# Optimization experiments

Hardware: AMD Instinct MI355X
Metric: run time of the kernel (lower is better)

## Reference

```python
import jax, jax.numpy as jnp
import numpy as np

H = 16
QK_NOPE = 128
QK_ROPE = 64
QK_HEAD = 192
V_HEAD = 128
KV_LORA = 512
Q_LORA = 1536
HIDDEN = 2048
ROPE_THETA = 500000.0
EPS = 1e-6


def _rms_norm(x, w, eps=EPS):
    var = jnp.mean(x * x, axis=-1, keepdims=True)
    return w * (x * jax.lax.rsqrt(var + eps))


def _rotate_half(x):
    d = x.shape[-1] // 2
    return jnp.concatenate([-x[..., d:], x[..., :d]], axis=-1)


def _rope_cos_sin(T, dim, theta, dtype):
    inv_freq = 1.0 / (theta ** (jnp.arange(0, dim, 2, dtype=jnp.float32) / dim))
    t = jnp.arange(T, dtype=jnp.float32)
    freqs = jnp.outer(t, inv_freq)               # [T, dim//2]
    emb = jnp.concatenate([freqs, freqs], axis=-1)  # [T, dim]
    return jnp.cos(emb).astype(dtype), jnp.sin(emb).astype(dtype)


def _apply_rope_interleave(q, k, cos, sin):
    # deinterleave: [x0,x1,x2,...] -> [x0,x2,... , x1,x3,...]
    def deint(x):
        return jnp.concatenate([x[..., 0::2], x[..., 1::2]], axis=-1)
    q, k = deint(q), deint(k)
    cos = cos[None, None]  # [1,1,T,d]
    sin = sin[None, None]
    q_e = q * cos + _rotate_half(q) * sin
    k_e = k * cos + _rotate_half(k) * sin
    return q_e, k_e


def setup_inputs() -> dict:
    key = jax.random.key(0)
    ks = jax.random.split(key, 8)
    s = 0.02
    B, T = 2, 2048
    return {
        "x": jax.random.normal(ks[0], (B, T, HIDDEN), jnp.float32),
        "q_a_w": jax.random.normal(ks[1], (HIDDEN, Q_LORA), jnp.float32) * s,
        "q_a_ln_w": jnp.ones((Q_LORA,), jnp.float32),
        "q_b_w": jax.random.normal(ks[2], (Q_LORA, H * QK_HEAD), jnp.float32) * s,
        "kv_a_w": jax.random.normal(ks[3], (HIDDEN, KV_LORA + QK_ROPE), jnp.float32) * s,
        "kv_a_ln_w": jnp.ones((KV_LORA,), jnp.float32),
        "kv_b_w": jax.random.normal(ks[4], (KV_LORA, H * (QK_NOPE + V_HEAD)), jnp.float32) * s,
        "o_w": jax.random.normal(ks[5], (H * V_HEAD, HIDDEN), jnp.float32) * s,
    }


def reference(x, q_a_w, q_a_ln_w, q_b_w, kv_a_w, kv_a_ln_w, kv_b_w, o_w):
    B, T, _ = x.shape
    scale = QK_HEAD ** -0.5

    # Q path: hidden -> q_lora -> RMSNorm -> H*qk_head
    q = _rms_norm(x @ q_a_w, q_a_ln_w) @ q_b_w
    q = q.reshape(B, T, H, QK_HEAD).transpose(0, 2, 1, 3)  # [B,H,T,qk_head]
    q_nope, q_rope = q[..., :QK_NOPE], q[..., QK_NOPE:]

    # KV path: hidden -> kv_lora + rope_dim
    ckv = x @ kv_a_w
    kv_c, k_rope = ckv[..., :KV_LORA], ckv[..., KV_LORA:]
    kv = _rms_norm(kv_c, kv_a_ln_w) @ kv_b_w
    kv = kv.reshape(B, T, H, QK_NOPE + V_HEAD).transpose(0, 2, 1, 3)
    k_nope, v = kv[..., :QK_NOPE], kv[..., QK_NOPE:]

    k_rope = k_rope.reshape(B, 1, T, QK_ROPE)
    cos, sin = _rope_cos_sin(T, QK_ROPE, ROPE_THETA, x.dtype)
    q_rope, k_rope = _apply_rope_interleave(q_rope, k_rope, cos, sin)
    k_rope = jnp.broadcast_to(k_rope, (B, H, T, QK_ROPE))

    qf = jnp.concatenate([q_nope, q_rope], axis=-1)  # [B,H,T,192]
    kf = jnp.concatenate([k_nope, k_rope], axis=-1)

    # causal SDPA
    scores = jnp.einsum("bhqd,bhkd->bhqk", qf, kf) * scale
    causal = jnp.tril(jnp.ones((T, T), bool))
    scores = jnp.where(causal[None, None], scores, jnp.finfo(scores.dtype).min)
    attn = jax.nn.softmax(scores, axis=-1)
    out = jnp.einsum("bhqk,bhkd->bhqd", attn, v)  # [B,H,T,128]
    out = out.transpose(0, 2, 1, 3).reshape(B, T, H * V_HEAD)
    return out @ o_w
```

## Files before the change

### kernel.cpp

```cpp
#include <hip/hip_runtime.h>
#include <hip/hip_bf16.h>
#include <cstdint>


typedef __bf16 bf16;
typedef __bf16 bf16x8 __attribute__((ext_vector_type(8)));
typedef __bf16 bf16x4v __attribute__((ext_vector_type(4)));
typedef float f32x4 __attribute__((ext_vector_type(4)));

#define TSEQ 2048
#define MR 4096

typedef const uint32_t __attribute__((address_space(1))) * gas1_t;
typedef uint32_t __attribute__((address_space(3))) * las3_t;

static __device__ __forceinline__ void gload_lds16(const void* g, void* l) {
  __builtin_amdgcn_global_load_lds(
      reinterpret_cast<gas1_t>(reinterpret_cast<uintptr_t>(g)),
      reinterpret_cast<las3_t>(reinterpret_cast<uintptr_t>(l)), 16, 0, 0);
}

static __device__ __forceinline__ f32x4 mfma16(bf16x8 a, bf16x8 b, f32x4 c) {
  return __builtin_amdgcn_mfma_f32_16x16x32_bf16(a, b, c, 0, 0, 0);
}

static __device__ __forceinline__ void do_transpose(
    const float* __restrict__ W, bf16* __restrict__ Wt, int K, int N, int bi,
    int bj, float (*t)[33]) {
  int c = threadIdx.x & 31, r0 = threadIdx.x >> 5;
#pragma unroll
  for (int rr = 0; rr < 32; rr += 8)
    t[rr + r0][c] = W[(size_t)(bj * 32 + rr + r0) * N + bi * 32 + c];
  __syncthreads();
#pragma unroll
  for (int rr = 0; rr < 32; rr += 8)
    Wt[(size_t)(bi * 32 + rr + r0) * K + bj * 32 + c] = (bf16)t[c][rr + r0];
}

#define PREP_BLOCKS (8192 + 3072 + 1152 + 4608 + 2048 + 4096 + 192 + 256)

__global__ __launch_bounds__(256) void k_prep(
    const float* __restrict__ x, const float* __restrict__ q_a_w,
    const float* __restrict__ kv_a_w, const float* __restrict__ q_b_w,
    const float* __restrict__ kv_b_w, const float* __restrict__ o_w,
    bf16* __restrict__ x_bf, bf16* __restrict__ ab_wt,
    bf16* __restrict__ qb_wt, bf16* __restrict__ kvb_wt,
    bf16* __restrict__ o_wt, float* __restrict__ rt) {
  __shared__ float t[32][33];
  int nb = blockIdx.x;
  const int tid = threadIdx.x;
  if (nb < 8192) {
    int i = nb * 256 + tid;
    float4 f = reinterpret_cast<const float4*>(x)[i];
    bf16x4v o = {(bf16)f.x, (bf16)f.y, (bf16)f.z, (bf16)f.w};
    reinterpret_cast<bf16x4v*>(x_bf)[i] = o;
    return;
  }
  nb -= 8192;
  if (nb < 3072) { do_transpose(q_a_w, ab_wt, 2048, 1536, nb % 48, nb / 48, t); return; }
  nb -= 3072;
  if (nb < 1152) {
    do_transpose(kv_a_w, ab_wt + (size_t)1536 * 2048, 2048, 576, nb % 18, nb / 18, t);
    return;
  }
  nb -= 1152;
  if (nb < 4608) { do_transpose(q_b_w, qb_wt, 1536, 3072, nb % 96, nb / 96, t); return; }
  nb -= 4608;
  if (nb < 2048) { do_transpose(kv_b_w, kvb_wt, 512, 4096, nb % 128, nb / 128, t); return; }
  nb -= 2048;
  if (nb < 4096) { do_transpose(o_w, o_wt, 2048, 2048, nb % 64, nb / 64, t); return; }
  nb -= 4096;
  if (nb < 192) {
    uint4 z = make_uint4(0, 0, 0, 0);
    reinterpret_cast<uint4*>(ab_wt + (size_t)2112 * 2048)[nb * 256 + tid] = z;
    return;
  }
  nb -= 192;
  {
    int idx = nb * 256 + tid;
    int tt = idx >> 5, j = idx & 31;
    float freq = exp2f(-(float)j * (1.0f / 32.0f) * log2f(500000.0f));
    float ang = (float)tt * freq;
    rt[tt * 64 + 2 * j] = cosf(ang);
    rt[tt * 64 + 2 * j + 1] = sinf(ang);
  }
}

__global__ __launch_bounds__(64) void k_norms(
    const bf16* __restrict__ qac, const float* __restrict__ qw,
    const float* __restrict__ kvw, const float* __restrict__ rt,
    bf16* __restrict__ q_a_n, bf16* __restrict__ kv_c_n,
    bf16* __restrict__ kr) {
  int row = blockIdx.x, lane = threadIdx.x;
  const bf16* ip = qac + (size_t)row * 2304;
  bf16x8 v[3];
  float ss = 0.f;
#pragma unroll
  for (int c = 0; c < 3; ++c) {
    v[c] = *reinterpret_cast<const bf16x8*>(ip + c * 512 + lane * 8);
#pragma unroll
    for (int e = 0; e < 8; ++e) { float f = (float)v[c][e]; ss += f * f; }
  }
#pragma unroll
  for (int m = 1; m <= 32; m <<= 1) ss += __shfl_xor(ss, m);
  float rs = rsqrtf(ss / 1536.0f + 1e-6f);
  bf16* op = q_a_n + (size_t)row * 1536;
#pragma unroll
  for (int c = 0; c < 3; ++c) {
    bf16x8 o;
#pragma unroll
    for (int e = 0; e < 8; ++e)
      o[e] = (bf16)((float)v[c][e] * rs * qw[c * 512 + lane * 8 + e]);
    *reinterpret_cast<bf16x8*>(op + c * 512 + lane * 8) = o;
  }
  bf16x8 kvv = *reinterpret_cast<const bf16x8*>(ip + 1536 + lane * 8);
  float s2 = 0.f;
#pragma unroll
  for (int e = 0; e < 8; ++e) { float f = (float)kvv[e]; s2 += f * f; }
#pragma unroll
  for (int m = 1; m <= 32; m <<= 1) s2 += __shfl_xor(s2, m);
  float rs2 = rsqrtf(s2 / 512.0f + 1e-6f);
  bf16x8 o2;
#pragma unroll
  for (int e = 0; e < 8; ++e)
    o2[e] = (bf16)((float)kvv[e] * rs2 * kvw[lane * 8 + e]);
  *reinterpret_cast<bf16x8*>(kv_c_n + (size_t)row * 512 + lane * 8) = o2;
  if (lane < 32) {
    int t = row & (TSEQ - 1);
    float x0 = (float)ip[2048 + 2 * lane], x1 = (float)ip[2048 + 2 * lane + 1];
    float c = rt[t * 64 + 2 * lane], s = rt[t * 64 + 2 * lane + 1];
    kr[(size_t)row * 64 + lane] = (bf16)(x0 * c - x1 * s);
    kr[(size_t)row * 64 + 32 + lane] = (bf16)(x1 * c + x0 * s);
  }
}

#define GPH(BUF, MH, KH, DO_READB, STAGE_STMT, WAIT_STMT)                     \
  {                                                                           \
    if (DO_READB) {                                                           \
      _Pragma("unroll") for (int ni = 0; ni < 4; ++ni) {                      \
        int row = wn * 64 + ni * 16 + lr;                                     \
        breg[KH][ni] = *reinterpret_cast<const bf16x8*>(                      \
            &Bs[BUF][row * 64 + ((((KH)*4 + lg) ^ (row & 7)) * 8)]);          \
      }                                                                       \
    }                                                                         \
    bf16x8 af[4];                                                             \
    _Pragma("unroll") for (int mi = 0; mi < 4; ++mi) {                        \
      int row = wm * 128 + (MH)*64 + mi * 16 + lr;                            \
      af[mi] = *reinterpret_cast<const bf16x8*>(                              \
          &As[BUF][row * 64 + ((((KH)*4 + lg) ^ (row & 7)) * 8)]);            \
    }                                                                         \
    STAGE_STMT;                                                               \
    __builtin_amdgcn_s_barrier();                                             \
    __builtin_amdgcn_s_setprio(1);                                            \
    _Pragma("unroll") for (int mi = 0; mi < 4; ++mi)                          \
        _Pragma("unroll") for (int ni = 0; ni < 4; ++ni)                      \
            acc[(MH)*4 + mi][ni] =                                            \
        mfma16(af[mi], breg[KH][ni], acc[(MH)*4 + mi][ni]);                   \
    __builtin_amdgcn_s_setprio(0);                                            \
    WAIT_STMT;                                                                \
    __builtin_amdgcn_s_barrier();                                             \
  }

template <bool OUT_F32>
static __device__ __forceinline__ void gemm8_body(
    const bf16* __restrict__ A, const bf16* __restrict__ Bt,
    void* __restrict__ C, int N, int K, int bi, int bj, bf16 (*As)[16384],
    bf16 (*Bs)[16384]) {
  const int tid = threadIdx.x, lane = tid & 63, w = tid >> 6;
  const int lg = lane >> 4, lr = lane & 15;
  const int wm = w >> 2, wn = w & 3;
  const int m0 = bj * 256, n0 = bi * 256;
  const int T = K >> 7;

  f32x4 acc[8][4] = {};
  bf16x8 breg[2][4];

  auto stageA = [&](int tau, int h) {
    char* dst = (char*)&As[tau & 1][0] + h * 16384;
#pragma unroll
    for (int j = 0; j < 2; ++j) {
      int c = j * 512 + tid;
      int row = c >> 3, slot = c & 7;
      gload_lds16(A + (size_t)(m0 + h * 128 + row) * K + tau * 64 +
                      ((slot ^ (row & 7)) * 8),
                  dst + (size_t)(j * 512 + w * 64) * 16);
    }
  };
  auto stageB = [&](int tau, int h) {
    char* dst = (char*)&Bs[tau & 1][0] + h * 16384;
#pragma unroll
    for (int j = 0; j < 2; ++j) {
      int c = j * 512 + tid;
      int row = c >> 3, slot = c & 7;
      gload_lds16(Bt + (size_t)(n0 + h * 128 + row) * K + tau * 64 +
                      ((slot ^ (row & 7)) * 8),
                  dst + (size_t)(j * 512 + w * 64) * 16);
    }
  };

  stageB(0, 0); stageB(0, 1); stageA(0, 0); stageA(0, 1);
  stageB(1, 0); stageB(1, 1); stageA(1, 0);
  asm volatile("s_waitcnt vmcnt(6)" ::: "memory");
  __builtin_amdgcn_s_barrier();

  for (int t = 0; t < T - 1; ++t) {
    const int s2 = 2 * t + 2, s3 = 2 * t + 3, a1 = 2 * t + 1;
    GPH(0, 0, 0, true,  stageA(a1, 1), ((void)0));
    GPH(0, 0, 1, true,  stageB(s2, 0), ((void)0));
    GPH(0, 1, 0, false, stageB(s2, 1), ((void)0));
    GPH(0, 1, 1, false, stageA(s2, 0),
        asm volatile("s_waitcnt vmcnt(6)" ::: "memory"));
    GPH(1, 0, 0, true,  stageA(s2, 1), ((void)0));
    GPH(1, 0, 1, true,  stageB(s3, 0), ((void)0));
    GPH(1, 1, 0, false, stageB(s3, 1), ((void)0));
    GPH(1, 1, 1, false, stageA(s3, 0),
        asm volatile("s_waitcnt vmcnt(6)" ::: "memory"));
  }
  {
    const int a1 = 2 * T - 1;
    GPH(0, 0, 0, true,  stageA(a1, 1), ((void)0));
    GPH(0, 0, 1, true,  ((void)0),     ((void)0));
    GPH(0, 1, 0, false, ((void)0),     ((void)0));
    GPH(0, 1, 1, false, ((void)0),
        asm volatile("s_waitcnt vmcnt(0)" ::: "memory"));
    GPH(1, 0, 0, true,  ((void)0), ((void)0));
    GPH(1, 0, 1, true,  ((void)0), ((void)0));
    GPH(1, 1, 0, false, ((void)0), ((void)0));
    GPH(1, 1, 1, false, ((void)0), ((void)0));
  }

#pragma unroll
  for (int mi = 0; mi < 8; ++mi)
#pragma unroll
    for (int ni = 0; ni < 4; ++ni) {
      int col = n0 + wn * 64 + ni * 16 + lr;
#pragma unroll
      for (int r = 0; r < 4; ++r) {
        int rowg = m0 + wm * 128 + mi * 16 + lg * 4 + r;
        if (OUT_F32)
          reinterpret_cast<float*>(C)[(size_t)rowg * N + col] = acc[mi][ni][r];
        else
          reinterpret_cast<bf16*>(C)[(size_t)rowg * N + col] =
              (bf16)acc[mi][ni][r];
      }
    }
}

template <bool OUT_F32>
__global__ __launch_bounds__(512, 2) void k_gemm8(const bf16* __restrict__ A,
                                                  const bf16* __restrict__ Bt,
                                                  void* __restrict__ C, int N,
                                                  int K) {
  __shared__ bf16 As[2][16384];
  __shared__ bf16 Bs[2][16384];
  const int nwg = gridDim.x * gridDim.y;
  const int orig = blockIdx.y * gridDim.x + blockIdx.x;
  const int wgid = (orig & 7) * (nwg >> 3) + (orig >> 3);
  gemm8_body<OUT_F32>(A, Bt, C, N, K, wgid % gridDim.x, wgid / gridDim.x, As,
                      Bs);
}

__global__ __launch_bounds__(512, 2) void k_gemm8_dual(
    const bf16* __restrict__ A1, const bf16* __restrict__ B1,
    bf16* __restrict__ C1, const bf16* __restrict__ A2,
    const bf16* __restrict__ B2, bf16* __restrict__ C2) {
  __shared__ bf16 As[2][16384];
  __shared__ bf16 Bs[2][16384];
  int id = blockIdx.x;
  if (id < 192) {
    int wg = (id & 7) * 24 + (id >> 3);
    gemm8_body<false>(A1, B1, C1, 3072, 1536, wg % 12, wg / 12, As, Bs);
  } else {
    int s = id - 192;
    int wg = (s & 7) * 32 + (s >> 3);
    gemm8_body<false>(A2, B2, C2, 4096, 512, wg % 16, wg / 16, As, Bs);
  }
}

#define GPN(BUF, KH, STAGE_STMT, WAIT_STMT)                                   \
  {                                                                           \
    bf16x8 bfr[4];                                                            \
    _Pragma("unroll") for (int ni = 0; ni < 4; ++ni) {                        \
      int row = wn * 64 + ni * 16 + lr;                                       \
      bfr[ni] = *reinterpret_cast<const bf16x8*>(                             \
          &Bs[BUF][row * 64 + ((((KH)*4 + lg) ^ (row & 7)) * 8)]);            \
    }                                                                         \
    bf16x8 af[4];                                                             \
    _Pragma("unroll") for (int mi = 0; mi < 4; ++mi) {                        \
      int row = wm * 64 + mi * 16 + lr;                                       \
      af[mi] = *reinterpret_cast<const bf16x8*>(                              \
          &As[BUF][row * 64 + ((((KH)*4 + lg) ^ (row & 7)) * 8)]);            \
    }                                                                         \
    STAGE_STMT;                                                               \
    __builtin_amdgcn_s_barrier();                                             \
    __builtin_amdgcn_s_setprio(1);                                            \
    _Pragma("unroll") for (int mi = 0; mi < 4; ++mi)                          \
        _Pragma("unroll") for (int ni = 0; ni < 4; ++ni)                      \
            acc[mi][ni] = mfma16(af[mi], bfr[ni], acc[mi][ni]);               \
    __builtin_amdgcn_s_setprio(0);                                            \
    WAIT_STMT;                                                                \
    __builtin_amdgcn_s_barrier();                                             \
  }

template <bool OUT_F32>
__global__ __launch_bounds__(512, 2) void k_gemm4n(const bf16* __restrict__ A,
                                                   const bf16* __restrict__ Bt,
                                                   void* __restrict__ C, int N,
                                                   int K) {
  __shared__ bf16 As[2][16384];
  __shared__ bf16 Bs[2][8192];
  const int tid = threadIdx.x, lane = tid & 63, w = tid >> 6;
  const int lg = lane >> 4, lr = lane & 15;
  const int wm = w >> 1, wn = w & 1;
  const int nwg = gridDim.x * gridDim.y;
  const int orig = blockIdx.y * gridDim.x + blockIdx.x;
  const int wgid = (orig & 7) * (nwg >> 3) + (orig >> 3);
  const int m0 = (wgid / gridDim.x) * 256, n0 = (wgid % gridDim.x) * 128;
  const int T = K >> 7;

  f32x4 acc[4][4] = {};

  auto stA = [&](int tau, int h) {
    char* dst = (char*)&As[tau & 1][0] + h * 16384;
#pragma unroll
    for (int j = 0; j < 2; ++j) {
      int c = j * 512 + tid;
      int row = c >> 3, slot = c & 7;
      gload_lds16(A + (size_t)(m0 + h * 128 + row) * K + tau * 64 +
                      ((slot ^ (row & 7)) * 8),
                  dst + (size_t)(j * 512 + w * 64) * 16);
    }
  };
  auto stB = [&](int tau) {
    char* dst = (char*)&Bs[tau & 1][0];
#pragma unroll
    for (int j = 0; j < 2; ++j) {
      int c = j * 512 + tid;
      int row = c >> 3, slot = c & 7;
      gload_lds16(Bt + (size_t)(n0 + row) * K + tau * 64 +
                      ((slot ^ (row & 7)) * 8),
                  dst + (size_t)(j * 512 + w * 64) * 16);
    }
  };

  stA(0, 0); stA(0, 1); stB(0); stA(1, 0);
  asm volatile("s_waitcnt vmcnt(2)" ::: "memory");
  __builtin_amdgcn_s_barrier();

  for (int t = 0; t < T - 1; ++t) {
    const int u1 = 2 * t + 1, s2 = 2 * t + 2, s3 = 2 * t + 3;
    GPN(0, 0, stA(u1, 1), ((void)0));
    GPN(0, 1, { stB(u1); stA(s2, 0); },
        asm volatile("s_waitcnt vmcnt(2)" ::: "memory"));
    GPN(1, 0, stA(s2, 1), ((void)0));
    GPN(1, 1, { stB(s2); stA(s3, 0); },
        asm volatile("s_waitcnt vmcnt(2)" ::: "memory"));
  }
  {
    const int u1 = 2 * T - 1;
    GPN(0, 0, stA(u1, 1), ((void)0));
    GPN(0, 1, stB(u1),
        asm volatile("s_waitcnt vmcnt(0)" ::: "memory"));
    GPN(1, 0, ((void)0), ((void)0));
    GPN(1, 1, ((void)0), ((void)0));
  }

#pragma unroll
  for (int mi = 0; mi < 4; ++mi)
#pragma unroll
    for (int ni = 0; ni < 4; ++ni) {
      int col = n0 + wn * 64 + ni * 16 + lr;
#pragma unroll
      for (int r = 0; r < 4; ++r) {
        int rowg = m0 + wm * 64 + mi * 16 + lg * 4 + r;
        if (OUT_F32)
          reinterpret_cast<float*>(C)[(size_t)rowg * N + col] = acc[mi][ni][r];
        else
          reinterpret_cast<bf16*>(C)[(size_t)rowg * N + col] =
              (bf16)acc[mi][ni][r];
      }
    }
}

__global__ __launch_bounds__(512, 2) void k_attn(const bf16* __restrict__ q,
                                                 const bf16* __restrict__ kv,
                                                 const bf16* __restrict__ kr,
                                                 const float* __restrict__ rt,
                                                 bf16* __restrict__ o) {
  __shared__ bf16 Kn[2][64 * 128];
  __shared__ bf16 Kr[2][64 * 64];
  __shared__ bf16 Vs[2][64 * 128];
  __shared__ bf16 Ps[8 * 1024];
  const int tid = threadIdx.x, lane = tid & 63, w = tid >> 6;
  const int lg = lane >> 4, lr = lane & 15;
  const float qsc = 0.07216878364870323f * 1.44269504088896f;
  uint4 vreg[2];
  const int vrr = tid & 31, vvc = tid >> 5;

  for (int t = 0; t < 2; ++t) {
    const int id = t ? 511 - (int)blockIdx.x : (int)blockIdx.x;
    const int qt = 15 - (id >> 5);
    const int bh = id & 31;
    const int b = bh >> 4, h = bh & 15;
    const int q0 = qt * 128;
    const size_t rowbase = (size_t)b * TSEQ;
    const int nkt = 2 * qt + 2;
    const int qg = q0 + w * 16 + lr;

    auto issue_loads = [&](int kbase, int buf) {
#pragma unroll
      for (int kk = 0; kk < 2; ++kk)
        vreg[kk] = *reinterpret_cast<const uint4*>(
            kv + (rowbase + kbase + vrr * 2 + kk) * 4096 + h * 256 + 128 +
            vvc * 8);
#pragma unroll
      for (int i = 0; i < 2; ++i) {
        int c = i * 512 + tid;
        int row = c >> 4, j = c & 15;
        gload_lds16(
            kv + (rowbase + kbase + row) * 4096 + h * 256 +
                ((j ^ (row & 15)) * 8),
            (char*)&Kn[buf][0] + (size_t)(i * 512 + w * 64) * 16);
      }
      {
        int row = tid >> 3, j = tid & 7;
        gload_lds16(kr + (rowbase + kbase + row) * 64 + ((j ^ (row & 7)) * 8),
                    (char*)&Kr[buf][0] + (size_t)(w * 64) * 16);
      }
    };

    auto write_vs = [&](int buf) {
      const int kb0 = vrr * 2;
      const int cC = kb0 >> 5, g = (kb0 >> 3) & 3, j0 = kb0 & 7;
      const uint32_t* r0 = reinterpret_cast<const uint32_t*>(&vreg[0]);
      const uint32_t* r1 = reinterpret_cast<const uint32_t*>(&vreg[1]);
#pragma unroll
      for (int e = 0; e < 8; ++e) {
        uint32_t h0 = (r0[e >> 1] >> ((e & 1) * 16)) & 0xffffu;
        uint32_t h1 = (r1[e >> 1] >> ((e & 1) * 16)) & 0xffffu;
        int vd = vvc * 8 + e;
        int slot = (vd & 15) ^ g;
        *reinterpret_cast<uint32_t*>(
            &Vs[buf][((cC * 8 + (vd >> 4)) * 4 + g) * 128 + slot * 8 + j0]) =
            h0 | (h1 << 16);
      }
    };

    bf16x8 qf[6];
    {
      const bf16* qp = q + (rowbase + qg) * 3072 + h * 192;
#pragma unroll
      for (int dc = 0; dc < 4; ++dc) {
        bf16x8 v = *reinterpret_cast<const bf16x8*>(qp + dc * 32 + lg * 8);
#pragma unroll
        for (int e = 0; e < 8; ++e) v[e] = (bf16)((float)v[e] * qsc);
        qf[dc] = v;
      }
      bf16x8 ra = *reinterpret_cast<const bf16x8*>(qp + 128 + lg * 16);
      bf16x8 rb = *reinterpret_cast<const bf16x8*>(qp + 128 + lg * 16 + 8);
      const float* rtp = rt + (size_t)qg * 64 + lg * 16;
      float4 r0 = *reinterpret_cast<const float4*>(rtp);
      float4 r1 = *reinterpret_cast<const float4*>(rtp + 4);
      float4 r2 = *reinterpret_cast<const float4*>(rtp + 8);
      float4 r3 = *reinterpret_cast<const float4*>(rtp + 12);
      float rc[8] = {r0.x, r0.z, r1.x, r1.z, r2.x, r2.z, r3.x, r3.z};
      float rs_[8] = {r0.y, r0.w, r1.y, r1.w, r2.y, r2.w, r3.y, r3.w};
      bf16x8 v4, v5;
#pragma unroll
      for (int j = 0; j < 8; ++j) {
        float x0 = (float)((j < 4) ? ra[2 * j] : rb[2 * j - 8]);
        float x1 = (float)((j < 4) ? ra[2 * j + 1] : rb[2 * j - 7]);
        v4[j] = (bf16)((x0 * rc[j] - x1 * rs_[j]) * qsc);
        v5[j] = (bf16)((x1 * rc[j] + x0 * rs_[j]) * qsc);
      }
      qf[4] = v4;
      qf[5] = v5;
    }

    f32x4 oacc[8] = {};
    float m_run = -1e30f, l_run = 0.f;

    issue_loads(0, 0);
    write_vs(0);
    __syncthreads();

    for (int kt = 0; kt < nkt; ++kt) {
      const int kbase = kt * 64;
      const int buf = kt & 1;
      const bool more = (kt + 1 < nkt);
      if (more) issue_loads(kbase + 64, buf ^ 1);

      if (kbase <= q0 + w * 16 + 15) {
        f32x4 sacc[4];
#pragma unroll
        for (int kb = 0; kb < 4; ++kb) {
          const int row = kb * 16 + lr;
          bf16x8 kf[6];
#pragma unroll
          for (int dc = 0; dc < 4; ++dc)
            kf[dc] = *reinterpret_cast<const bf16x8*>(
                &Kn[buf][row * 128 + (((dc * 4 + lg) ^ (row & 15)) * 8)]);
#pragma unroll
          for (int dc = 0; dc < 2; ++dc)
            kf[4 + dc] = *reinterpret_cast<const bf16x8*>(
                &Kr[buf][row * 64 + (((dc * 4 + lg) ^ (row & 7)) * 8)]);
          __builtin_amdgcn_s_setprio(1);
          f32x4 sa = {0.f, 0.f, 0.f, 0.f};
#pragma unroll
          for (int dc = 0; dc < 6; ++dc) sa = mfma16(kf[dc], qf[dc], sa);
          sacc[kb] = sa;
          __builtin_amdgcn_s_setprio(0);
        }
        float sv[4][4];
        if (kbase + 63 <= q0 + w * 16) {
#pragma unroll
          for (int kb = 0; kb < 4; ++kb)
#pragma unroll
            for (int r = 0; r < 4; ++r) sv[kb][r] = sacc[kb][r];
        } else {
#pragma unroll
          for (int kb = 0; kb < 4; ++kb)
#pragma unroll
            for (int r = 0; r < 4; ++r) {
              int kgl = kbase + kb * 16 + lg * 4 + r;
              sv[kb][r] = (kgl <= qg) ? sacc[kb][r] : -1e30f;
            }
        }
        float pmax = -1e30f;
#pragma unroll
        for (int kb = 0; kb < 4; ++kb)
#pragma unroll
          for (int r = 0; r < 4; ++r) pmax = fmaxf(pmax, sv[kb][r]);
        pmax = fmaxf(pmax, __shfl_xor(pmax, 16));
        pmax = fmaxf(pmax, __shfl_xor(pmax, 32));
        if (!__all(pmax - m_run <= 8.0f)) {
          float mnew = fmaxf(m_run, pmax);
          float alpha = exp2f(m_run - mnew);
          l_run *= alpha;
#pragma unroll
          for (int vb = 0; vb < 8; ++vb) {
            oacc[vb][0] *= alpha; oacc[vb][1] *= alpha;
            oacc[vb][2] *= alpha; oacc[vb][3] *= alpha;
          }
          m_run = mnew;
        }
        float ls = 0.f;
#pragma unroll
        for (int kb = 0; kb < 4; ++kb) {
          bf16x4v pw;
#pragma unroll
          for (int r = 0; r < 4; ++r) {
            float p = exp2f(sv[kb][r] - m_run);
            ls += p;
            pw[r] = (bf16)p;
          }
          *reinterpret_cast<bf16x4v*>(
              &Ps[w * 1024 + lr * 64 +
                  (((kb * 2 + (lg >> 1)) ^ (lr & 7)) * 8) + (lg & 1) * 4]) = pw;
        }
        ls += __shfl_xor(ls, 16);
        ls += __shfl_xor(ls, 32);
        l_run += ls;
#pragma unroll
        for (int c = 0; c < 2; ++c) {
          bf16x8 pb = *reinterpret_cast<const bf16x8*>(
              &Ps[w * 1024 + lr * 64 + (((c * 4 + lg) ^ (lr & 7)) * 8)]);
          __builtin_amdgcn_s_setprio(1);
#pragma unroll
          for (int vb = 0; vb < 8; ++vb) {
            bf16x8 av = *reinterpret_cast<const bf16x8*>(
                &Vs[buf][((c * 8 + vb) * 4 + lg) * 128 + (lr ^ lg) * 8]);
            oacc[vb] = mfma16(av, pb, oacc[vb]);
          }
          __builtin_amdgcn_s_setprio(0);
        }
      }
      if (more) write_vs(buf ^ 1);
      __syncthreads();
    }

    bf16* Os = &Kn[0][0] + w * 2048;
    {
      float inv = 1.0f / l_run;
#pragma unroll
      for (int vb = 0; vb < 8; ++vb) {
        bf16x4v ov;
#pragma unroll
        for (int r = 0; r < 4; ++r) ov[r] = (bf16)(oacc[vb][r] * inv);
        int slot16 = vb * 2 + (lg >> 1);
        *reinterpret_cast<bf16x4v*>(
            &Os[lr * 128 + ((slot16 ^ (lr & 7)) * 8) + (lg & 1) * 4]) = ov;
      }
    }
    asm volatile("s_waitcnt lgkmcnt(0)");
    __builtin_amdgcn_sched_barrier(0);
#pragma unroll
    for (int i = 0; i < 4; ++i) {
      const int r = i * 4 + lg;
      bf16x8 ov = *reinterpret_cast<const bf16x8*>(
          &Os[r * 128 + ((lr ^ (r & 7)) * 8)]);
      *reinterpret_cast<bf16x8*>(
          o + (rowbase + q0 + w * 16 + r) * 2048 + h * 128 + lr * 8) = ov;
    }
    __syncthreads();
  }
}

extern "C" void kernel_launch(void* const* d_in, const int* in_sizes, int n_in,
                              void* d_out, int out_size, void* d_ws,
                              size_t ws_size, hipStream_t stream) {
  (void)in_sizes; (void)n_in; (void)out_size; (void)ws_size;
  const float* x       = (const float*)d_in[0];
  const float* q_a_w   = (const float*)d_in[1];
  const float* q_a_ln  = (const float*)d_in[2];
  const float* q_b_w   = (const float*)d_in[3];
  const float* kv_a_w  = (const float*)d_in[4];
  const float* kv_a_ln = (const float*)d_in[5];
  const float* kv_b_w  = (const float*)d_in[6];
  const float* o_w     = (const float*)d_in[7];

  char* ws = (char*)d_ws;
  size_t off = 0;
  auto alloc = [&](size_t bytes) {
    void* p = ws + off;
    off += (bytes + 255) & ~(size_t)255;
    return p;
  };
  bf16* x_bf   = (bf16*)alloc((size_t)MR * 2048 * 2);
  bf16* ab_wt  = (bf16*)alloc((size_t)2304 * 2048 * 2);
  bf16* qb_wt  = (bf16*)alloc((size_t)3072 * 1536 * 2);
  bf16* kvb_wt = (bf16*)alloc((size_t)4096 * 512 * 2);
  bf16* o_wt   = (bf16*)alloc((size_t)2048 * 2048 * 2);
  float* rt    = (float*)alloc((size_t)2048 * 64 * 4);
  bf16* qac    = (bf16*)alloc((size_t)MR * 2304 * 2);
  bf16* q_a_n  = (bf16*)alloc((size_t)MR * 1536 * 2);
  bf16* kv_c_n = (bf16*)alloc((size_t)MR * 512 * 2);
  bf16* kr     = (bf16*)alloc((size_t)MR * 64 * 2);
  bf16* qbuf   = (bf16*)alloc((size_t)MR * 3072 * 2);
  bf16* kvbuf  = (bf16*)alloc((size_t)MR * 4096 * 2);
  bf16* attn_o = (bf16*)alloc((size_t)MR * 2048 * 2);

  k_prep<<<PREP_BLOCKS, 256, 0, stream>>>(x, q_a_w, kv_a_w, q_b_w, kv_b_w,
                                          o_w, x_bf, ab_wt, qb_wt, kvb_wt,
                                          o_wt, rt);
  k_gemm8<false><<<dim3(9, 16), 512, 0, stream>>>(x_bf, ab_wt, qac, 2304, 2048);
  k_norms<<<MR, 64, 0, stream>>>(qac, q_a_ln, kv_a_ln, rt, q_a_n, kv_c_n, kr);
  k_gemm8_dual<<<dim3(448), 512, 0, stream>>>(q_a_n, qb_wt, qbuf, kv_c_n,
                                              kvb_wt, kvbuf);
  k_attn<<<dim3(256), 512, 0, stream>>>(qbuf, kvbuf, kr, rt, attn_o);
  k_gemm4n<true><<<dim3(16, 16), 512, 0, stream>>>(attn_o, o_wt, d_out, 2048,
                                                   2048);
}
```

Baseline: 259.7 us.

## Replace 256x256 GEMM tiles with smaller tiles for projection GEMMs

Removes the 256x256-tile GEMM kernel. The first projection GEMM now uses a new 128x128-tile kernel on an 18x32 grid, and the dual q_b/kv_b GEMM now uses 256x128 tiles across 896 blocks. The aim is to fix wave quantization and undersubscription on the many CUs of MI355X, since the old grids of 144 and 448 workgroups left CUs idle. The cost is lower arithmetic intensity per tile, which means more global and LDS traffic per FLOP.

```diff
diff --git a/kernel.cpp b/kernel.cpp
--- a/kernel.cpp
+++ b/kernel.cpp
@@ -131,149 +131,6 @@
     float c = rt[t * 64 + 2 * lane], s = rt[t * 64 + 2 * lane + 1];
     kr[(size_t)row * 64 + lane] = (bf16)(x0 * c - x1 * s);
     kr[(size_t)row * 64 + 32 + lane] = (bf16)(x1 * c + x0 * s);
-  }
-}
-
-#define GPH(BUF, MH, KH, DO_READB, STAGE_STMT, WAIT_STMT)                     \
-  {                                                                           \
-    if (DO_READB) {                                                           \
-      _Pragma("unroll") for (int ni = 0; ni < 4; ++ni) {                      \
-        int row = wn * 64 + ni * 16 + lr;                                     \
-        breg[KH][ni] = *reinterpret_cast<const bf16x8*>(                      \
-            &Bs[BUF][row * 64 + ((((KH)*4 + lg) ^ (row & 7)) * 8)]);          \
-      }                                                                       \
-    }                                                                         \
-    bf16x8 af[4];                                                             \
-    _Pragma("unroll") for (int mi = 0; mi < 4; ++mi) {                        \
-      int row = wm * 128 + (MH)*64 + mi * 16 + lr;                            \
-      af[mi] = *reinterpret_cast<const bf16x8*>(                              \
-          &As[BUF][row * 64 + ((((KH)*4 + lg) ^ (row & 7)) * 8)]);            \
-    }                                                                         \
-    STAGE_STMT;                                                               \
-    __builtin_amdgcn_s_barrier();                                             \
-    __builtin_amdgcn_s_setprio(1);                                            \
-    _Pragma("unroll") for (int mi = 0; mi < 4; ++mi)                          \
-        _Pragma("unroll") for (int ni = 0; ni < 4; ++ni)                      \
-            acc[(MH)*4 + mi][ni] =                                            \
-        mfma16(af[mi], breg[KH][ni], acc[(MH)*4 + mi][ni]);                   \
-    __builtin_amdgcn_s_setprio(0);                                            \
-    WAIT_STMT;                                                                \
-    __builtin_amdgcn_s_barrier();                                             \
-  }
-
-template <bool OUT_F32>
-static __device__ __forceinline__ void gemm8_body(
-    const bf16* __restrict__ A, const bf16* __restrict__ Bt,
-    void* __restrict__ C, int N, int K, int bi, int bj, bf16 (*As)[16384],
-    bf16 (*Bs)[16384]) {
-  const int tid = threadIdx.x, lane = tid & 63, w = tid >> 6;
-  const int lg = lane >> 4, lr = lane & 15;
-  const int wm = w >> 2, wn = w & 3;
-  const int m0 = bj * 256, n0 = bi * 256;
-  const int T = K >> 7;
-
-  f32x4 acc[8][4] = {};
-  bf16x8 breg[2][4];
-
-  auto stageA = [&](int tau, int h) {
-    char* dst = (char*)&As[tau & 1][0] + h * 16384;
-#pragma unroll
-    for (int j = 0; j < 2; ++j) {
-      int c = j * 512 + tid;
-      int row = c >> 3, slot = c & 7;
-      gload_lds16(A + (size_t)(m0 + h * 128 + row) * K + tau * 64 +
-                      ((slot ^ (row & 7)) * 8),
-                  dst + (size_t)(j * 512 + w * 64) * 16);
-    }
-  };
-  auto stageB = [&](int tau, int h) {
-    char* dst = (char*)&Bs[tau & 1][0] + h * 16384;
-#pragma unroll
-    for (int j = 0; j < 2; ++j) {
-      int c = j * 512 + tid;
-      int row = c >> 3, slot = c & 7;
-      gload_lds16(Bt + (size_t)(n0 + h * 128 + row) * K + tau * 64 +
-                      ((slot ^ (row & 7)) * 8),
-                  dst + (size_t)(j * 512 + w * 64) * 16);
-    }
-  };
-
-  stageB(0, 0); stageB(0, 1); stageA(0, 0); stageA(0, 1);
-  stageB(1, 0); stageB(1, 1); stageA(1, 0);
-  asm volatile("s_waitcnt vmcnt(6)" ::: "memory");
-  __builtin_amdgcn_s_barrier();
-
-  for (int t = 0; t < T - 1; ++t) {
-    const int s2 = 2 * t + 2, s3 = 2 * t + 3, a1 = 2 * t + 1;
-    GPH(0, 0, 0, true,  stageA(a1, 1), ((void)0));
-    GPH(0, 0, 1, true,  stageB(s2, 0), ((void)0));
-    GPH(0, 1, 0, false, stageB(s2, 1), ((void)0));
-    GPH(0, 1, 1, false, stageA(s2, 0),
-        asm volatile("s_waitcnt vmcnt(6)" ::: "memory"));
-    GPH(1, 0, 0, true,  stageA(s2, 1), ((void)0));
-    GPH(1, 0, 1, true,  stageB(s3, 0), ((void)0));
-    GPH(1, 1, 0, false, stageB(s3, 1), ((void)0));
-    GPH(1, 1, 1, false, stageA(s3, 0),
-        asm volatile("s_waitcnt vmcnt(6)" ::: "memory"));
-  }
-  {
-    const int a1 = 2 * T - 1;
-    GPH(0, 0, 0, true,  stageA(a1, 1), ((void)0));
-    GPH(0, 0, 1, true,  ((void)0),     ((void)0));
-    GPH(0, 1, 0, false, ((void)0),     ((void)0));
-    GPH(0, 1, 1, false, ((void)0),
-        asm volatile("s_waitcnt vmcnt(0)" ::: "memory"));
-    GPH(1, 0, 0, true,  ((void)0), ((void)0));
-    GPH(1, 0, 1, true,  ((void)0), ((void)0));
-    GPH(1, 1, 0, false, ((void)0), ((void)0));
-    GPH(1, 1, 1, false, ((void)0), ((void)0));
-  }
-
-#pragma unroll
-  for (int mi = 0; mi < 8; ++mi)
-#pragma unroll
-    for (int ni = 0; ni < 4; ++ni) {
-      int col = n0 + wn * 64 + ni * 16 + lr;
-#pragma unroll
-      for (int r = 0; r < 4; ++r) {
-        int rowg = m0 + wm * 128 + mi * 16 + lg * 4 + r;
-        if (OUT_F32)
-          reinterpret_cast<float*>(C)[(size_t)rowg * N + col] = acc[mi][ni][r];
-        else
-          reinterpret_cast<bf16*>(C)[(size_t)rowg * N + col] =
-              (bf16)acc[mi][ni][r];
-      }
-    }
-}
-
-template <bool OUT_F32>
-__global__ __launch_bounds__(512, 2) void k_gemm8(const bf16* __restrict__ A,
-                                                  const bf16* __restrict__ Bt,
-                                                  void* __restrict__ C, int N,
-                                                  int K) {
-  __shared__ bf16 As[2][16384];
-  __shared__ bf16 Bs[2][16384];
-  const int nwg = gridDim.x * gridDim.y;
-  const int orig = blockIdx.y * gridDim.x + blockIdx.x;
-  const int wgid = (orig & 7) * (nwg >> 3) + (orig >> 3);
-  gemm8_body<OUT_F32>(A, Bt, C, N, K, wgid % gridDim.x, wgid / gridDim.x, As,
-                      Bs);
-}
-
-__global__ __launch_bounds__(512, 2) void k_gemm8_dual(
-    const bf16* __restrict__ A1, const bf16* __restrict__ B1,
-    bf16* __restrict__ C1, const bf16* __restrict__ A2,
-    const bf16* __restrict__ B2, bf16* __restrict__ C2) {
-  __shared__ bf16 As[2][16384];
-  __shared__ bf16 Bs[2][16384];
-  int id = blockIdx.x;
-  if (id < 192) {
-    int wg = (id & 7) * 24 + (id >> 3);
-    gemm8_body<false>(A1, B1, C1, 3072, 1536, wg % 12, wg / 12, As, Bs);
-  } else {
-    int s = id - 192;
-    int wg = (s & 7) * 32 + (s >> 3);
-    gemm8_body<false>(A2, B2, C2, 4096, 512, wg % 16, wg / 16, As, Bs);
   }
 }
 
@@ -303,19 +160,14 @@
   }
 
 template <bool OUT_F32>
-__global__ __launch_bounds__(512, 2) void k_gemm4n(const bf16* __restrict__ A,
-                                                   const bf16* __restrict__ Bt,
-                                                   void* __restrict__ C, int N,
-                                                   int K) {
-  __shared__ bf16 As[2][16384];
-  __shared__ bf16 Bs[2][8192];
+static __device__ __forceinline__ void gemm4n_body(
+    const bf16* __restrict__ A, const bf16* __restrict__ Bt,
+    void* __restrict__ C, int N, int K, int bi, int bj, bf16 (*As)[16384],
+    bf16 (*Bs)[8192]) {
   const int tid = threadIdx.x, lane = tid & 63, w = tid >> 6;
   const int lg = lane >> 4, lr = lane & 15;
   const int wm = w >> 1, wn = w & 1;
-  const int nwg = gridDim.x * gridDim.y;
-  const int orig = blockIdx.y * gridDim.x + blockIdx.x;
-  const int wgid = (orig & 7) * (nwg >> 3) + (orig >> 3);
-  const int m0 = (wgid / gridDim.x) * 256, n0 = (wgid % gridDim.x) * 128;
+  const int m0 = bj * 256, n0 = bi * 128;
   const int T = K >> 7;
 
   f32x4 acc[4][4] = {};
@@ -373,6 +225,142 @@
 #pragma unroll
       for (int r = 0; r < 4; ++r) {
         int rowg = m0 + wm * 64 + mi * 16 + lg * 4 + r;
+        if (OUT_F32)
+          reinterpret_cast<float*>(C)[(size_t)rowg * N + col] = acc[mi][ni][r];
+        else
+          reinterpret_cast<bf16*>(C)[(size_t)rowg * N + col] =
+              (bf16)acc[mi][ni][r];
+      }
+    }
+}
+
+template <bool OUT_F32>
+__global__ __launch_bounds__(512, 2) void k_gemm4n(const bf16* __restrict__ A,
+                                                   const bf16* __restrict__ Bt,
+                                                   void* __restrict__ C, int N,
+                                                   int K) {
+  __shared__ bf16 As[2][16384];
+  __shared__ bf16 Bs[2][8192];
+  const int nwg = gridDim.x * gridDim.y;
+  const int orig = blockIdx.y * gridDim.x + blockIdx.x;
+  const int wgid = (orig & 7) * (nwg >> 3) + (orig >> 3);
+  gemm4n_body<OUT_F32>(A, Bt, C, N, K, wgid % gridDim.x, wgid / gridDim.x, As,
+                       Bs);
+}
+
+__global__ __launch_bounds__(512, 2) void k_gemm4n_dual(
+    const bf16* __restrict__ A1, const bf16* __restrict__ B1,
+    bf16* __restrict__ C1, const bf16* __restrict__ A2,
+    const bf16* __restrict__ B2, bf16* __restrict__ C2) {
+  __shared__ bf16 As[2][16384];
+  __shared__ bf16 Bs[2][8192];
+  int id = blockIdx.x;
+  if (id < 384) {
+    int wg = (id & 7) * 48 + (id >> 3);
+    gemm4n_body<false>(A1, B1, C1, 3072, 1536, wg % 24, wg / 24, As, Bs);
+  } else {
+    int s = id - 384;
+    int wg = (s & 7) * 64 + (s >> 3);
+    gemm4n_body<false>(A2, B2, C2, 4096, 512, wg % 32, wg / 32, As, Bs);
+  }
+}
+
+#define GPS(BUF, KH, STAGE_STMT, WAIT_STMT)                                   \
+  {                                                                           \
+    bf16x8 bfr[4];                                                            \
+    _Pragma("unroll") for (int ni = 0; ni < 4; ++ni) {                        \
+      int row = wc * 64 + ni * 16 + lr;                                       \
+      bfr[ni] = *reinterpret_cast<const bf16x8*>(                             \
+          &Bs[BUF][row * 64 + ((((KH)*4 + lg) ^ (row & 7)) * 8)]);            \
+    }                                                                         \
+    bf16x8 af[2];                                                             \
+    _Pragma("unroll") for (int mi = 0; mi < 2; ++mi) {                        \
+      int row = wr * 32 + mi * 16 + lr;                                       \
+      af[mi] = *reinterpret_cast<const bf16x8*>(                              \
+          &As[BUF][row * 64 + ((((KH)*4 + lg) ^ (row & 7)) * 8)]);            \
+    }                                                                         \
+    STAGE_STMT;                                                               \
+    __builtin_amdgcn_s_barrier();                                             \
+    __builtin_amdgcn_s_setprio(1);                                            \
+    _Pragma("unroll") for (int mi = 0; mi < 2; ++mi)                          \
+        _Pragma("unroll") for (int ni = 0; ni < 4; ++ni)                      \
+            acc[mi][ni] = mfma16(af[mi], bfr[ni], acc[mi][ni]);               \
+    __builtin_amdgcn_s_setprio(0);                                            \
+    WAIT_STMT;                                                                \
+    __builtin_amdgcn_s_barrier();                                             \
+  }
+
+template <bool OUT_F32>
+__global__ __launch_bounds__(512, 2) void k_gemm2s(const bf16* __restrict__ A,
+                                                   const bf16* __restrict__ Bt,
+                                                   void* __restrict__ C, int N,
+                                                   int K) {
+  __shared__ bf16 As[2][8192];
+  __shared__ bf16 Bs[2][8192];
+  const int tid = threadIdx.x, lane = tid & 63, w = tid >> 6;
+  const int lg = lane >> 4, lr = lane & 15;
+  const int wr = w >> 1, wc = w & 1;
+  const int nwg = gridDim.x * gridDim.y;
+  const int orig = blockIdx.y * gridDim.x + blockIdx.x;
+  const int wgid = (orig & 7) * (nwg >> 3) + (orig >> 3);
+  const int m0 = (wgid / gridDim.x) * 128, n0 = (wgid % gridDim.x) * 128;
+  const int T = K >> 7;
+
+  f32x4 acc[2][4] = {};
+
+  auto stA = [&](int tau) {
+    char* dst = (char*)&As[tau & 1][0];
+#pragma unroll
+    for (int j = 0; j < 2; ++j) {
+      int c = j * 512 + tid;
+      int row = c >> 3, slot = c & 7;
+      gload_lds16(A + (size_t)(m0 + row) * K + tau * 64 +
+                      ((slot ^ (row & 7)) * 8),
+                  dst + (size_t)(j * 512 + w * 64) * 16);
+    }
+  };
+  auto stB = [&](int tau) {
+    char* dst = (char*)&Bs[tau & 1][0];
+#pragma unroll
+    for (int j = 0; j < 2; ++j) {
+      int c = j * 512 + tid;
+      int row = c >> 3, slot = c & 7;
+      gload_lds16(Bt + (size_t)(n0 + row) * K + tau * 64 +
+                      ((slot ^ (row & 7)) * 8),
+                  dst + (size_t)(j * 512 + w * 64) * 16);
+    }
+  };
+
+  stA(0); stB(0); stA(1);
+  asm volatile("s_waitcnt vmcnt(2)" ::: "memory");
+  __builtin_amdgcn_s_barrier();
+
+  for (int t = 0; t < T - 1; ++t) {
+    const int u1 = 2 * t + 1, s2 = 2 * t + 2, s3 = 2 * t + 3;
+    GPS(0, 0, stB(u1), ((void)0));
+    GPS(0, 1, stA(s2),
+        asm volatile("s_waitcnt vmcnt(2)" ::: "memory"));
+    GPS(1, 0, stB(s2), ((void)0));
+    GPS(1, 1, stA(s3),
+        asm volatile("s_waitcnt vmcnt(2)" ::: "memory"));
+  }
+  {
+    const int u1 = 2 * T - 1;
+    GPS(0, 0, stB(u1), ((void)0));
+    GPS(0, 1, ((void)0),
+        asm volatile("s_waitcnt vmcnt(0)" ::: "memory"));
+    GPS(1, 0, ((void)0), ((void)0));
+    GPS(1, 1, ((void)0), ((void)0));
+  }
+
+#pragma unroll
+  for (int mi = 0; mi < 2; ++mi)
+#pragma unroll
+    for (int ni = 0; ni < 4; ++ni) {
+      int col = n0 + wc * 64 + ni * 16 + lr;
+#pragma unroll
+      for (int r = 0; r < 4; ++r) {
+        int rowg = m0 + wr * 32 + mi * 16 + lg * 4 + r;
         if (OUT_F32)
           reinterpret_cast<float*>(C)[(size_t)rowg * N + col] = acc[mi][ni][r];
         else
@@ -643,10 +631,11 @@
   k_prep<<<PREP_BLOCKS, 256, 0, stream>>>(x, q_a_w, kv_a_w, q_b_w, kv_b_w,
                                           o_w, x_bf, ab_wt, qb_wt, kvb_wt,
                                           o_wt, rt);
-  k_gemm8<false><<<dim3(9, 16), 512, 0, stream>>>(x_bf, ab_wt, qac, 2304, 2048);
+  k_gemm2s<false><<<dim3(18, 32), 512, 0, stream>>>(x_bf, ab_wt, qac, 2304,
+                                                    2048);
   k_norms<<<MR, 64, 0, stream>>>(qac, q_a_ln, kv_a_ln, rt, q_a_n, kv_c_n, kr);
-  k_gemm8_dual<<<dim3(448), 512, 0, stream>>>(q_a_n, qb_wt, qbuf, kv_c_n,
-                                              kvb_wt, kvbuf);
+  k_gemm4n_dual<<<dim3(896), 512, 0, stream>>>(q_a_n, qb_wt, qbuf, kv_c_n,
+                                               kvb_wt, kvbuf);
   k_attn<<<dim3(256), 512, 0, stream>>>(qbuf, kvbuf, kr, rt, attn_o);
   k_gemm4n<true><<<dim3(16, 16), 512, 0, stream>>>(attn_o, o_wt, d_out, 2048,
                                                    2048);
```

Result: no change. 261.7 us (+0.8%).
